# Kernel tuning notes

Measured on AMD Instinct MI355X. Metric: run time of the kernel, lower is better.

The kernel has to match this reference:

```python
import jax, jax.numpy as jnp
import numpy as np

N = 50000      # nodes
E = 1600000    # edges
IN = 128       # in_features
OUT = 64       # out_features
H = 2          # heads
ALPHA = 0.2    # LeakyReLU negative slope


def setup_inputs() -> dict:
    key = jax.random.key(0)
    k1, k2, k3, k4 = jax.random.split(key, 4)
    x = jax.random.normal(k1, (N, IN), dtype=jnp.float32)
    edge_index = jax.random.randint(k2, (2, E), 0, N, dtype=jnp.int32)
    # xavier-uniform-ish scaled params
    W = jax.random.normal(k3, (H, IN, OUT), dtype=jnp.float32) / np.float32(np.sqrt(IN))
    a = jax.random.normal(k4, (H, 2 * OUT, 1), dtype=jnp.float32) * np.float32(0.1)
    return {"x": x, "W": W, "a": a, "edge_index": edge_index}


def reference(x, W, a, edge_index):
    src = edge_index[0]
    dst = edge_index[1]
    # per-head linear transform: [N, H, O]
    Wh = jnp.einsum('ni,hio->nho', x, W)
    # split attention vector: a @ [Wh_i || Wh_j] == Wh_i@a_i + Wh_j@a_j
    a_i = a[:, :OUT, 0]   # [H, O]
    a_j = a[:, OUT:, 0]   # [H, O]
    s_i = jnp.einsum('nho,ho->nh', Wh, a_i)   # [N, H]
    s_j = jnp.einsum('nho,ho->nh', Wh, a_j)   # [N, H]
    # per-edge attention logits, LeakyReLU
    e = jax.nn.leaky_relu(s_i[src] + s_j[dst], negative_slope=ALPHA)  # [E, H]
    # faithful to source: GLOBAL softmax over all edges (dim=0) per head
    attn = jax.nn.softmax(e, axis=0)  # [E, H]
    # dropout with rate 0.0 -> identity (eval mode)
    msg = attn[:, :, None] * Wh[dst]  # [E, H, O]
    h = jax.ops.segment_sum(msg, dst, num_segments=N)  # [N, H, O]
    # concat heads along feature dim
    return h.reshape(N, H * OUT)
```

## Files before the change

kernel.cpp:

```cpp
#include <hip/hip_runtime.h>

#define NN 50000
#define EE 1600000
#define INF 128
#define OUTF 64
#define NH 2
#define ALPHA 0.2f

#define RNG 16
#define NPR (NN / RNG)
#define NBB 250
#define EPB (EE / NBB)
#define BCAP 640
#define NBNODE 196
#define HCH 25
#define SPB (NBB / HCH)

typedef __attribute__((ext_vector_type(8))) short s16x8;
typedef __attribute__((ext_vector_type(4))) float f32x4;

__device__ __forceinline__ unsigned short bf16_rne(float f) {
    union { float f; unsigned u; } v; v.f = f;
    unsigned r = v.u + 0x7FFFu + ((v.u >> 16) & 1u);
    return (unsigned short)(r >> 16);
}
__device__ __forceinline__ float bf16_val(unsigned short h) {
    union { unsigned u; float f; } v; v.u = ((unsigned)h) << 16;
    return v.f;
}
__device__ __forceinline__ void split8(const float4 a, const float4 b,
                                       s16x8& hi, s16x8& lo) {
    const float p[8] = {a.x, a.y, a.z, a.w, b.x, b.y, b.z, b.w};
    #pragma unroll
    for (int j = 0; j < 8; ++j) {
        const unsigned short h = bf16_rne(p[j]);
        hi[j] = (short)h;
        lo[j] = (short)bf16_rne(p[j] - bf16_val(h));
    }
}


__global__ __launch_bounds__(512)
void gat_node(const float* __restrict__ x, const float* __restrict__ Wg,
              const float* __restrict__ av, const int* __restrict__ ei,
              float* __restrict__ out, float* __restrict__ si,
              float* __restrict__ sj, unsigned* __restrict__ buckets,
              int* __restrict__ counts, float* __restrict__ Z)
{
    __shared__ unsigned short WsL[36864];
    __shared__ int cnt[16];
    const int tid = threadIdx.x;

    if (blockIdx.x < NBB) {
        const int bid = blockIdx.x;
        if (bid == 0 && tid < 2) Z[tid] = 0.0f;
        if (tid < 16) cnt[tid] = 0;
        __syncthreads();
        const int e0 = bid * EPB;
        for (int i = tid; i < EPB / 4; i += 512) {
            const int4 s4 = *(const int4*)&ei[e0 + 4 * i];
            const int4 d4 = *(const int4*)&ei[EE + e0 + 4 * i];
            const int ss[4] = {s4.x, s4.y, s4.z, s4.w};
            const int dd[4] = {d4.x, d4.y, d4.z, d4.w};
            #pragma unroll
            for (int k = 0; k < 4; ++k) {
                const int r = dd[k] / NPR;
                const int rel = dd[k] - r * NPR;
                const int pos = atomicAdd(&cnt[r], 1);
                if (pos < BCAP)
                    buckets[(size_t)(r * NBB + bid) * BCAP + pos] =
                        (unsigned)ss[k] | ((unsigned)rel << 16);
            }
        }
        __syncthreads();
        if (tid < 16) counts[tid * NBB + bid] = min(cnt[tid], BCAP);
        return;
    }

    const int bx = blockIdx.x - NBB;
    const int lane = tid & 63;
    const int wv = tid >> 6;
    const int lm = lane & 15;
    const int quad = lane >> 4;

    for (int idx = tid; idx < 16384; idx += 512) {
        const int h = idx >> 13;
        const int k = (idx >> 6) & 127;
        const int o = idx & 63;
        const float w = Wg[idx];
        const unsigned short hi = bf16_rne(w);
        const unsigned short lo = bf16_rne(w - bf16_val(hi));
        const int n  = h * 64 + o;
        const int nt = n >> 4;
        const int ks = k >> 5;
        const int kk = k & 31;
        const int ln = (kk >> 3) * 16 + (n & 15);
        const int pos = ((nt * 4 + ks) * 64 + ln) * 8 + (kk & 7);
        WsL[pos] = hi;
        WsL[18432 + pos] = lo;
    }
    for (int i = tid; i < 2048; i += 512) {
        WsL[16384 + i] = 0;
        WsL[18432 + 16384 + i] = 0;
    }
    __syncthreads();
    if (tid < 128) {
        const int k = tid;
        float u0 = 0.f, u1 = 0.f, u2 = 0.f, u3 = 0.f;
        #pragma unroll 4
        for (int o = 0; o < 64; o += 4) {
            const float4 w0 = *(const float4*)&Wg[k * 64 + o];
            const float4 w1 = *(const float4*)&Wg[8192 + k * 64 + o];
            const float4 ai0 = *(const float4*)&av[o];
            const float4 aj0 = *(const float4*)&av[64 + o];
            const float4 ai1 = *(const float4*)&av[128 + o];
            const float4 aj1 = *(const float4*)&av[192 + o];
            u0 += w0.x*ai0.x + w0.y*ai0.y + w0.z*ai0.z + w0.w*ai0.w;
            u1 += w0.x*aj0.x + w0.y*aj0.y + w0.z*aj0.z + w0.w*aj0.w;
            u2 += w1.x*ai1.x + w1.y*ai1.y + w1.z*ai1.z + w1.w*ai1.w;
            u3 += w1.x*aj1.x + w1.y*aj1.y + w1.z*aj1.z + w1.w*aj1.w;
        }
        const float uu[4] = {u0, u1, u2, u3};
        const int ks = k >> 5;
        const int kk = k & 31;
        #pragma unroll
        for (int n = 0; n < 4; ++n) {
            const int ln = (kk >> 3) * 16 + n;
            const int pos = ((32 + ks) * 64 + ln) * 8 + (kk & 7);
            const unsigned short hi = bf16_rne(uu[n]);
            WsL[pos] = hi;
            WsL[18432 + pos] = bf16_rne(uu[n] - bf16_val(hi));
        }
    }

    const int rowA0 = bx * 256 + wv * 32 + lm;
    const int rowA1 = rowA0 + 16;
    const int rc0 = rowA0 < NN ? rowA0 : NN - 1;
    const int rc1 = rowA1 < NN ? rowA1 : NN - 1;
    const float* xp0 = x + (size_t)rc0 * INF + quad * 8;
    const float* xp1 = x + (size_t)rc1 * INF + quad * 8;

    f32x4 acc[2][9];
    #pragma unroll
    for (int mi = 0; mi < 2; ++mi)
        #pragma unroll
        for (int nt = 0; nt < 9; ++nt) acc[mi][nt] = (f32x4)0.0f;

    __syncthreads();

    #pragma unroll
    for (int ks = 0; ks < 4; ++ks) {
        s16x8 ah0, al0, ah1, al1;
        {
            const float4 u0 = *(const float4*)(xp0 + ks * 32);
            const float4 v0 = *(const float4*)(xp0 + ks * 32 + 4);
            split8(u0, v0, ah0, al0);
            const float4 u1 = *(const float4*)(xp1 + ks * 32);
            const float4 v1 = *(const float4*)(xp1 + ks * 32 + 4);
            split8(u1, v1, ah1, al1);
        }
        #pragma unroll
        for (int nt = 0; nt < 9; ++nt) {
            const s16x8 bh = *(const s16x8*)&WsL[((nt * 4 + ks) * 64 + lane) * 8];
            const s16x8 bl = *(const s16x8*)&WsL[18432 + ((nt * 4 + ks) * 64 + lane) * 8];
            acc[0][nt] = __builtin_amdgcn_mfma_f32_16x16x32_bf16(ah0, bh, acc[0][nt], 0, 0, 0);
            acc[0][nt] = __builtin_amdgcn_mfma_f32_16x16x32_bf16(ah0, bl, acc[0][nt], 0, 0, 0);
            acc[0][nt] = __builtin_amdgcn_mfma_f32_16x16x32_bf16(al0, bh, acc[0][nt], 0, 0, 0);
            acc[1][nt] = __builtin_amdgcn_mfma_f32_16x16x32_bf16(ah1, bh, acc[1][nt], 0, 0, 0);
            acc[1][nt] = __builtin_amdgcn_mfma_f32_16x16x32_bf16(ah1, bl, acc[1][nt], 0, 0, 0);
            acc[1][nt] = __builtin_amdgcn_mfma_f32_16x16x32_bf16(al1, bh, acc[1][nt], 0, 0, 0);
        }
    }

    #pragma unroll
    for (int mi = 0; mi < 2; ++mi) {
        const int rowb = bx * 256 + wv * 32 + mi * 16 + quad * 4;
        #pragma unroll
        for (int r = 0; r < 4; ++r) {
            const int rr = rowb + r;
            if (rr < NN) {
                const float sv = acc[mi][8][r];
                if (lm == 0)      si[2 * rr] = sv;
                else if (lm == 1) sj[2 * rr] = sv;
                else if (lm == 2) si[2 * rr + 1] = sv;
                else if (lm == 3) sj[2 * rr + 1] = sv;
                float* orow = out + (size_t)rr * (NH * OUTF) + lm;
                #pragma unroll
                for (int nt = 0; nt < 8; ++nt) orow[nt * 16] = acc[mi][nt][r];
            }
        }
    }
}

__global__ __launch_bounds__(512)
void gat_hist(const unsigned* __restrict__ buckets, const int* __restrict__ counts,
              const float* __restrict__ si, const float* __restrict__ sj,
              float* __restrict__ partial, float* __restrict__ Z)
{
    __shared__ float bins[NPR * 2];
    __shared__ float zr0[8], zr1[8];
    const int c = blockIdx.x;
    const int r = blockIdx.y;
    const int nlo = r * NPR;

    for (int i = threadIdx.x; i < NPR; i += 512)
        ((float2*)bins)[i] = make_float2(0.f, 0.f);
    __syncthreads();

    float z0 = 0.f, z1 = 0.f;
    #pragma unroll
    for (int bb = 0; bb < SPB; ++bb) {
        const int b = c * SPB + bb;
        const int n = counts[r * NBB + b];
        const uint4* seg4 = (const uint4*)(buckets + (size_t)(r * NBB + b) * BCAP);
        const int n4 = (n + 3) >> 2;
        for (int i = threadIdx.x; i < n4; i += 512) {
            const uint4 pk4 = seg4[i];
            const unsigned pks[4] = {pk4.x, pk4.y, pk4.z, pk4.w};
            #pragma unroll
            for (int j = 0; j < 4; ++j) {
                if (4 * i + j < n) {
                    const unsigned pk = pks[j];
                    const int s = (int)(pk & 0xFFFFu);
                    const int rel = (int)(pk >> 16);
                    const float2 vi = *(const float2*)&si[2 * s];
                    const float2 vj = *(const float2*)&sj[2 * (nlo + rel)];
                    float a0 = vi.x + vj.x; a0 = a0 > 0.f ? a0 : ALPHA * a0;
                    float a1 = vi.y + vj.y; a1 = a1 > 0.f ? a1 : ALPHA * a1;
                    const float w0 = expf(a0);
                    const float w1 = expf(a1);
                    atomicAdd(&bins[2 * rel], w0);
                    atomicAdd(&bins[2 * rel + 1], w1);
                    z0 += w0; z1 += w1;
                }
            }
        }
    }

    #pragma unroll
    for (int m = 1; m < 64; m <<= 1) {
        z0 += __shfl_xor(z0, m, 64);
        z1 += __shfl_xor(z1, m, 64);
    }
    const int wv = threadIdx.x >> 6;
    if ((threadIdx.x & 63) == 0) { zr0[wv] = z0; zr1[wv] = z1; }
    __syncthreads();
    if (threadIdx.x == 0) {
        float t0 = 0.f, t1 = 0.f;
        #pragma unroll
        for (int i = 0; i < 8; ++i) { t0 += zr0[i]; t1 += zr1[i]; }
        atomicAdd(&Z[0], t0);
        atomicAdd(&Z[1], t1);
    }

    float2* P = (float2*)(partial + (size_t)c * 100000 + nlo * 2);
    for (int i = threadIdx.x; i < NPR; i += 512)
        P[i] = ((const float2*)bins)[i];
}

__global__ __launch_bounds__(256)
void gat_scale(float* __restrict__ out, const float* __restrict__ partial,
               const float* __restrict__ Z)
{
    __shared__ float sc[256];
    const int tid = threadIdx.x;
    const int n0 = blockIdx.x * 128;
    const float rz0 = 1.0f / Z[0];
    const float rz1 = 1.0f / Z[1];

    const int nvals = min(256, 100000 - n0 * 2);
    if (tid < nvals) {
        float ssum = 0.f;
        #pragma unroll 5
        for (int c = 0; c < HCH; ++c)
            ssum += partial[(size_t)c * 100000 + n0 * 2 + tid];
        sc[tid] = ssum * ((tid & 1) ? rz1 : rz0);
    }
    __syncthreads();

    float4* ob = (float4*)(out + (size_t)n0 * 128);
    const int lim4 = min(128, NN - n0) * 32;
    for (int i = tid; i < lim4; i += 256) {
        const int row = i >> 5;
        const int c4 = i & 31;
        const float s = sc[row * 2 + (c4 >> 4)];
        float4 v = ob[i];
        v.x *= s; v.y *= s; v.z *= s; v.w *= s;
        ob[i] = v;
    }
}

extern "C" void kernel_launch(void* const* d_in, const int* in_sizes, int n_in,
                              void* d_out, int out_size, void* d_ws, size_t ws_size,
                              hipStream_t stream)
{
    const float* x = (const float*)d_in[0];
    const float* W = (const float*)d_in[1];
    const float* a = (const float*)d_in[2];
    const int* ei = (const int*)d_in[3];
    float* out = (float*)d_out;
    float* ws = (float*)d_ws;

    float* si = ws;
    float* sj = ws + 100000;
    float* Z = ws + 200000;
    int* counts = (int*)(ws + 200016);
    unsigned* buckets = (unsigned*)(ws + 204032);
    float* partial = ws + 2764032;

    gat_node<<<dim3(NBB + NBNODE), dim3(512), 0, stream>>>(x, W, a, ei, out, si, sj,
                                                           buckets, counts, Z);

    gat_hist<<<dim3(HCH, RNG), dim3(512), 0, stream>>>(buckets, counts, si, sj,
                                                       partial, Z);

    gat_scale<<<dim3((NN + 127) / 128), dim3(256), 0, stream>>>(out, partial, Z);
}
```

Before: 151.8 us.

## Defer feature GEMM to final kernel and fuse softmax scaling into its epilogue

Splits the work so a first prep kernel computes only the attention scores si/sj (via a folded W·a vector and FMA plus shuffle reductions), buckets the edges, and pre-swizzles W into a split-bf16 layout in global memory. The MFMA GEMM for Wh now runs in the last kernel, where it reduces the per-node partial histograms and multiplies by 1/Z before writing the output once. This removes the separate scale pass, which re-read and re-wrote the full output. Bucket and histogram parameters change as well (fewer, larger bucket blocks with 16 histogram chunks). The cost is that x is read twice, and bucket capacity could overflow if any bucket gets more than 2048 edges.

```diff
diff --git a/kernel.cpp b/kernel.cpp
--- a/kernel.cpp
+++ b/kernel.cpp
@@ -9,11 +9,13 @@
 
 #define RNG 16
 #define NPR (NN / RNG)
-#define NBB 250
+#define NBB 64
 #define EPB (EE / NBB)
-#define BCAP 640
-#define NBNODE 196
-#define HCH 25
+#define BCAP 2048
+#define NSPREP 391
+#define NWPREP 64
+#define NBNODE 391
+#define HCH 16
 #define SPB (NBB / HCH)
 
 typedef __attribute__((ext_vector_type(8))) short s16x8;
@@ -40,24 +42,43 @@
 }
 
 
-__global__ __launch_bounds__(512)
-void gat_node(const float* __restrict__ x, const float* __restrict__ Wg,
+__global__ __launch_bounds__(256)
+void gat_prep(const float* __restrict__ x, const float* __restrict__ Wg,
               const float* __restrict__ av, const int* __restrict__ ei,
-              float* __restrict__ out, float* __restrict__ si,
-              float* __restrict__ sj, unsigned* __restrict__ buckets,
+              float* __restrict__ si, float* __restrict__ sj,
+              unsigned short* __restrict__ Wf, unsigned* __restrict__ buckets,
               int* __restrict__ counts, float* __restrict__ Z)
 {
-    __shared__ unsigned short WsL[36864];
+    __shared__ float4 u4[128];
     __shared__ int cnt[16];
     const int tid = threadIdx.x;
 
-    if (blockIdx.x < NBB) {
-        const int bid = blockIdx.x;
-        if (bid == 0 && tid < 2) Z[tid] = 0.0f;
+    if (blockIdx.x >= NSPREP + NBB) {
+        const int idx = (blockIdx.x - (NSPREP + NBB)) * 256 + tid;
+        if (idx < 2) Z[idx] = 0.0f;
+        const int h = idx >> 13;
+        const int k = (idx >> 6) & 127;
+        const int o = idx & 63;
+        const float w = Wg[idx];
+        const unsigned short hi = bf16_rne(w);
+        const unsigned short lo = bf16_rne(w - bf16_val(hi));
+        const int n  = h * 64 + o;
+        const int nt = n >> 4;
+        const int ks = k >> 5;
+        const int kk = k & 31;
+        const int ln = (kk >> 3) * 16 + (n & 15);
+        const int pos = ((nt * 4 + ks) * 64 + ln) * 8 + (kk & 7);
+        Wf[pos] = hi;
+        Wf[16384 + pos] = lo;
+        return;
+    }
+
+    if (blockIdx.x >= NSPREP) {
+        const int bid = blockIdx.x - NSPREP;
         if (tid < 16) cnt[tid] = 0;
         __syncthreads();
         const int e0 = bid * EPB;
-        for (int i = tid; i < EPB / 4; i += 512) {
+        for (int i = tid; i < EPB / 4; i += 256) {
             const int4 s4 = *(const int4*)&ei[e0 + 4 * i];
             const int4 d4 = *(const int4*)&ei[EE + e0 + 4 * i];
             const int ss[4] = {s4.x, s4.y, s4.z, s4.w};
@@ -77,33 +98,6 @@
         return;
     }
 
-    const int bx = blockIdx.x - NBB;
-    const int lane = tid & 63;
-    const int wv = tid >> 6;
-    const int lm = lane & 15;
-    const int quad = lane >> 4;
-
-    for (int idx = tid; idx < 16384; idx += 512) {
-        const int h = idx >> 13;
-        const int k = (idx >> 6) & 127;
-        const int o = idx & 63;
-        const float w = Wg[idx];
-        const unsigned short hi = bf16_rne(w);
-        const unsigned short lo = bf16_rne(w - bf16_val(hi));
-        const int n  = h * 64 + o;
-        const int nt = n >> 4;
-        const int ks = k >> 5;
-        const int kk = k & 31;
-        const int ln = (kk >> 3) * 16 + (n & 15);
-        const int pos = ((nt * 4 + ks) * 64 + ln) * 8 + (kk & 7);
-        WsL[pos] = hi;
-        WsL[18432 + pos] = lo;
-    }
-    for (int i = tid; i < 2048; i += 512) {
-        WsL[16384 + i] = 0;
-        WsL[18432 + 16384 + i] = 0;
-    }
-    __syncthreads();
     if (tid < 128) {
         const int k = tid;
         float u0 = 0.f, u1 = 0.f, u2 = 0.f, u3 = 0.f;
@@ -120,74 +114,41 @@
             u2 += w1.x*ai1.x + w1.y*ai1.y + w1.z*ai1.z + w1.w*ai1.w;
             u3 += w1.x*aj1.x + w1.y*aj1.y + w1.z*aj1.z + w1.w*aj1.w;
         }
-        const float uu[4] = {u0, u1, u2, u3};
-        const int ks = k >> 5;
-        const int kk = k & 31;
-        #pragma unroll
-        for (int n = 0; n < 4; ++n) {
-            const int ln = (kk >> 3) * 16 + n;
-            const int pos = ((32 + ks) * 64 + ln) * 8 + (kk & 7);
-            const unsigned short hi = bf16_rne(uu[n]);
-            WsL[pos] = hi;
-            WsL[18432 + pos] = bf16_rne(uu[n] - bf16_val(hi));
-        }
-    }
-
-    const int rowA0 = bx * 256 + wv * 32 + lm;
-    const int rowA1 = rowA0 + 16;
-    const int rc0 = rowA0 < NN ? rowA0 : NN - 1;
-    const int rc1 = rowA1 < NN ? rowA1 : NN - 1;
-    const float* xp0 = x + (size_t)rc0 * INF + quad * 8;
-    const float* xp1 = x + (size_t)rc1 * INF + quad * 8;
-
-    f32x4 acc[2][9];
-    #pragma unroll
-    for (int mi = 0; mi < 2; ++mi)
-        #pragma unroll
-        for (int nt = 0; nt < 9; ++nt) acc[mi][nt] = (f32x4)0.0f;
-
+        u4[k] = make_float4(u0, u1, u2, u3);
+    }
     __syncthreads();
 
-    #pragma unroll
-    for (int ks = 0; ks < 4; ++ks) {
-        s16x8 ah0, al0, ah1, al1;
-        {
-            const float4 u0 = *(const float4*)(xp0 + ks * 32);
-            const float4 v0 = *(const float4*)(xp0 + ks * 32 + 4);
-            split8(u0, v0, ah0, al0);
-            const float4 u1 = *(const float4*)(xp1 + ks * 32);
-            const float4 v1 = *(const float4*)(xp1 + ks * 32 + 4);
-            split8(u1, v1, ah1, al1);
-        }
-        #pragma unroll
-        for (int nt = 0; nt < 9; ++nt) {
-            const s16x8 bh = *(const s16x8*)&WsL[((nt * 4 + ks) * 64 + lane) * 8];
-            const s16x8 bl = *(const s16x8*)&WsL[18432 + ((nt * 4 + ks) * 64 + lane) * 8];
-            acc[0][nt] = __builtin_amdgcn_mfma_f32_16x16x32_bf16(ah0, bh, acc[0][nt], 0, 0, 0);
-            acc[0][nt] = __builtin_amdgcn_mfma_f32_16x16x32_bf16(ah0, bl, acc[0][nt], 0, 0, 0);
-            acc[0][nt] = __builtin_amdgcn_mfma_f32_16x16x32_bf16(al0, bh, acc[0][nt], 0, 0, 0);
-            acc[1][nt] = __builtin_amdgcn_mfma_f32_16x16x32_bf16(ah1, bh, acc[1][nt], 0, 0, 0);
-            acc[1][nt] = __builtin_amdgcn_mfma_f32_16x16x32_bf16(ah1, bl, acc[1][nt], 0, 0, 0);
-            acc[1][nt] = __builtin_amdgcn_mfma_f32_16x16x32_bf16(al1, bh, acc[1][nt], 0, 0, 0);
-        }
-    }
-
-    #pragma unroll
-    for (int mi = 0; mi < 2; ++mi) {
-        const int rowb = bx * 256 + wv * 32 + mi * 16 + quad * 4;
-        #pragma unroll
-        for (int r = 0; r < 4; ++r) {
-            const int rr = rowb + r;
-            if (rr < NN) {
-                const float sv = acc[mi][8][r];
-                if (lm == 0)      si[2 * rr] = sv;
-                else if (lm == 1) sj[2 * rr] = sv;
-                else if (lm == 2) si[2 * rr + 1] = sv;
-                else if (lm == 3) sj[2 * rr + 1] = sv;
-                float* orow = out + (size_t)rr * (NH * OUTF) + lm;
-                #pragma unroll
-                for (int nt = 0; nt < 8; ++nt) orow[nt * 16] = acc[mi][nt][r];
-            }
+    const int lane = tid & 63;
+    const int wv = tid >> 6;
+    const int lm = lane & 15;
+    const int rsub = lane >> 4;
+
+    #pragma unroll
+    for (int p = 0; p < 8; ++p) {
+        const int row = blockIdx.x * 128 + p * 16 + wv * 4 + rsub;
+        const int rc = row < NN ? row : NN - 1;
+        const float4 xa = *(const float4*)(x + (size_t)rc * INF + lm * 8);
+        const float4 xb = *(const float4*)(x + (size_t)rc * INF + lm * 8 + 4);
+        float s0 = 0.f, s1 = 0.f, s2 = 0.f, s3 = 0.f;
+        const float xv[8] = {xa.x, xa.y, xa.z, xa.w, xb.x, xb.y, xb.z, xb.w};
+        #pragma unroll
+        for (int j = 0; j < 8; ++j) {
+            const float4 u = u4[lm * 8 + j];
+            s0 = fmaf(xv[j], u.x, s0);
+            s1 = fmaf(xv[j], u.y, s1);
+            s2 = fmaf(xv[j], u.z, s2);
+            s3 = fmaf(xv[j], u.w, s3);
+        }
+        #pragma unroll
+        for (int m = 1; m < 16; m <<= 1) {
+            s0 += __shfl_xor(s0, m, 64);
+            s1 += __shfl_xor(s1, m, 64);
+            s2 += __shfl_xor(s2, m, 64);
+            s3 += __shfl_xor(s3, m, 64);
+        }
+        if (lm == 0 && row < NN) {
+            *(float2*)&si[2 * row] = make_float2(s0, s2);
+            *(float2*)&sj[2 * row] = make_float2(s1, s3);
         }
     }
 }
@@ -259,34 +220,90 @@
 }
 
 __global__ __launch_bounds__(256)
-void gat_scale(float* __restrict__ out, const float* __restrict__ partial,
-               const float* __restrict__ Z)
+void gat_node(const float* __restrict__ x, const unsigned short* __restrict__ Wf,
+              const float* __restrict__ partial, const float* __restrict__ Z,
+              float* __restrict__ out)
 {
-    __shared__ float sc[256];
+    __shared__ unsigned short WsL[32768];
     const int tid = threadIdx.x;
-    const int n0 = blockIdx.x * 128;
+    const int lane = tid & 63;
+    const int wv = tid >> 6;
+    const int lm = lane & 15;
+    const int quad = lane >> 4;
+
+    {
+        const float4* gsrc = (const float4*)Wf;
+        float4* ldst = (float4*)WsL;
+        #pragma unroll
+        for (int i = 0; i < 16; ++i)
+            ldst[i * 256 + tid] = gsrc[i * 256 + tid];
+    }
+
     const float rz0 = 1.0f / Z[0];
     const float rz1 = 1.0f / Z[1];
 
-    const int nvals = min(256, 100000 - n0 * 2);
-    if (tid < nvals) {
-        float ssum = 0.f;
-        #pragma unroll 5
-        for (int c = 0; c < HCH; ++c)
-            ssum += partial[(size_t)c * 100000 + n0 * 2 + tid];
-        sc[tid] = ssum * ((tid & 1) ? rz1 : rz0);
-    }
+    const int rowA0 = blockIdx.x * 128 + wv * 32 + lm;
+    const int rowA1 = rowA0 + 16;
+    const int rc0 = rowA0 < NN ? rowA0 : NN - 1;
+    const int rc1 = rowA1 < NN ? rowA1 : NN - 1;
+    const float* xp0 = x + (size_t)rc0 * INF + quad * 8;
+    const float* xp1 = x + (size_t)rc1 * INF + quad * 8;
+
+    f32x4 acc[2][8];
+    #pragma unroll
+    for (int mi = 0; mi < 2; ++mi)
+        #pragma unroll
+        for (int nt = 0; nt < 8; ++nt) acc[mi][nt] = (f32x4)0.0f;
+
     __syncthreads();
 
-    float4* ob = (float4*)(out + (size_t)n0 * 128);
-    const int lim4 = min(128, NN - n0) * 32;
-    for (int i = tid; i < lim4; i += 256) {
-        const int row = i >> 5;
-        const int c4 = i & 31;
-        const float s = sc[row * 2 + (c4 >> 4)];
-        float4 v = ob[i];
-        v.x *= s; v.y *= s; v.z *= s; v.w *= s;
-        ob[i] = v;
+    #pragma unroll
+    for (int ks = 0; ks < 4; ++ks) {
+        s16x8 ah0, al0, ah1, al1;
+        {
+            const float4 u0 = *(const float4*)(xp0 + ks * 32);
+            const float4 v0 = *(const float4*)(xp0 + ks * 32 + 4);
+            split8(u0, v0, ah0, al0);
+            const float4 u1 = *(const float4*)(xp1 + ks * 32);
+            const float4 v1 = *(const float4*)(xp1 + ks * 32 + 4);
+            split8(u1, v1, ah1, al1);
+        }
+        #pragma unroll
+        for (int nt = 0; nt < 8; ++nt) {
+            const s16x8 bh = *(const s16x8*)&WsL[((nt * 4 + ks) * 64 + lane) * 8];
+            const s16x8 bl = *(const s16x8*)&WsL[16384 + ((nt * 4 + ks) * 64 + lane) * 8];
+            acc[0][nt] = __builtin_amdgcn_mfma_f32_16x16x32_bf16(ah0, bh, acc[0][nt], 0, 0, 0);
+            acc[0][nt] = __builtin_amdgcn_mfma_f32_16x16x32_bf16(ah0, bl, acc[0][nt], 0, 0, 0);
+            acc[0][nt] = __builtin_amdgcn_mfma_f32_16x16x32_bf16(al0, bh, acc[0][nt], 0, 0, 0);
+            acc[1][nt] = __builtin_amdgcn_mfma_f32_16x16x32_bf16(ah1, bh, acc[1][nt], 0, 0, 0);
+            acc[1][nt] = __builtin_amdgcn_mfma_f32_16x16x32_bf16(ah1, bl, acc[1][nt], 0, 0, 0);
+            acc[1][nt] = __builtin_amdgcn_mfma_f32_16x16x32_bf16(al1, bh, acc[1][nt], 0, 0, 0);
+        }
+    }
+
+    #pragma unroll
+    for (int mi = 0; mi < 2; ++mi) {
+        const int rowb = blockIdx.x * 128 + wv * 32 + mi * 16 + quad * 4;
+        #pragma unroll
+        for (int r = 0; r < 4; ++r) {
+            const int rr = rowb + r;
+            const int rrc = rr < NN ? rr : NN - 1;
+            float v0 = partial[(size_t)lm * 100000 + 2 * rrc];
+            float v1 = partial[(size_t)lm * 100000 + 2 * rrc + 1];
+            #pragma unroll
+            for (int m = 1; m < 16; m <<= 1) {
+                v0 += __shfl_xor(v0, m, 64);
+                v1 += __shfl_xor(v1, m, 64);
+            }
+            const float sc0 = v0 * rz0;
+            const float sc1 = v1 * rz1;
+            if (rr < NN) {
+                float* orow = out + (size_t)rr * (NH * OUTF) + lm;
+                #pragma unroll
+                for (int nt = 0; nt < 8; ++nt)
+                    orow[nt * 16] = acc[mi][nt][r] * (nt < 4 ? sc0 : sc1);
+            }
+        }
     }
 }
 
@@ -305,14 +322,15 @@
     float* sj = ws + 100000;
     float* Z = ws + 200000;
     int* counts = (int*)(ws + 200016);
-    unsigned* buckets = (unsigned*)(ws + 204032);
-    float* partial = ws + 2764032;
-
-    gat_node<<<dim3(NBB + NBNODE), dim3(512), 0, stream>>>(x, W, a, ei, out, si, sj,
-                                                           buckets, counts, Z);
+    unsigned short* Wf = (unsigned short*)(ws + 201056);
+    unsigned* buckets = (unsigned*)(ws + 217472);
+    float* partial = ws + 2314624;
+
+    gat_prep<<<dim3(NSPREP + NBB + NWPREP), dim3(256), 0, stream>>>(
+        x, W, a, ei, si, sj, Wf, buckets, counts, Z);
 
     gat_hist<<<dim3(HCH, RNG), dim3(512), 0, stream>>>(buckets, counts, si, sj,
                                                        partial, Z);
 
-    gat_scale<<<dim3((NN + 127) / 128), dim3(256), 0, stream>>>(out, partial, Z);
-}
+    gat_node<<<dim3(NBNODE), dim3(256), 0, stream>>>(x, Wf, partial, Z, out);
+}
```

Result: faster. 145.1 us (-4.4%).
